# Performance work log

Hardware: AMD Instinct MI355X
Metric: run time of the kernel (lower is better)

The kernel has to match this reference:

```python
import jax, jax.numpy as jnp
import numpy as np

N_USERS = 100000
N_ITEMS = 50000
N = N_USERS + N_ITEMS
NNZ = 2400000
D = 64
L = 3
B = 16384


def setup_inputs() -> dict:
    key = jax.random.key(0)
    ks = jax.random.split(key, 12)
    return {
        "user_emb": jax.random.normal(ks[0], (N_USERS, D), jnp.float32) * 0.1,
        "item_emb": jax.random.normal(ks[1], (N_ITEMS, D), jnp.float32) * 0.1,
        "W_gc": jax.random.normal(ks[2], (L, D, D), jnp.float32) * 0.1,
        "b_gc": jax.random.normal(ks[3], (L, 1, D), jnp.float32) * 0.1,
        "W_bi": jax.random.normal(ks[4], (L, D, D), jnp.float32) * 0.1,
        "b_bi": jax.random.normal(ks[5], (L, 1, D), jnp.float32) * 0.1,
        "adj_vals": jax.random.uniform(ks[6], (NNZ,), jnp.float32) * (1.0 / 16.0),
        "adj_rows": jax.random.randint(ks[7], (NNZ,), 0, N, jnp.int32),
        "adj_cols": jax.random.randint(ks[8], (NNZ,), 0, N, jnp.int32),
        "u": jax.random.randint(ks[9], (B,), 0, N_USERS, jnp.int32),
        "i": jax.random.randint(ks[10], (B,), 0, N_ITEMS, jnp.int32),
        "j": jax.random.randint(ks[11], (B,), 0, N_ITEMS, jnp.int32),
    }


def reference(user_emb, item_emb, W_gc, b_gc, W_bi, b_bi, adj_vals, adj_rows, adj_cols, u, i, j):
    n_users = user_emb.shape[0]
    n_nodes = n_users + item_emb.shape[0]
    ego = jnp.concatenate([user_emb, item_emb], axis=0)  # [N, D]
    all_emb = [ego]
    n_layers = W_gc.shape[0]
    for l in range(n_layers):
        # spmm: side = A_hat @ ego  (edge-list gather + weighted segment sum)
        gathered = ego[adj_cols] * adj_vals[:, None]            # [nnz, D]
        side = jax.ops.segment_sum(gathered, adj_rows, num_segments=n_nodes)  # [N, D]
        # graph-conv branch
        sum_emb = jax.nn.leaky_relu(side @ W_gc[l] + b_gc[l], 0.2)
        # bi-interaction branch
        bi_emb = jax.nn.leaky_relu((ego * side) @ W_bi[l] + b_bi[l], 0.2)
        ego = sum_emb + bi_emb
        # L2 normalize per node (F.normalize, eps=1e-12)
        norm = ego / jnp.maximum(jnp.linalg.norm(ego, axis=1, keepdims=True), 1e-12)
        all_emb.append(norm)
    final = jnp.concatenate(all_emb, axis=1)  # [N, D*(L+1)]
    u_g = final[u]
    i_g = final[n_users + i]
    j_g = final[n_users + j]
    return u_g, i_g, j_g
```

## Files before the change

### kernel.cpp

```cpp
#include <hip/hip_runtime.h>

#define DD 64
#define RB 256
#define RB_SHIFT 8
#define CAP 4608
#define NBLKA 512
#define NBLKA_SHIFT 9
#define BMAX 1024
#define COLM 0x3FFFF
#define WT_STRIDE 80
#define EMAX 4704
#define SPAD 68

typedef __attribute__((ext_vector_type(8))) short bf16x8;
typedef __attribute__((ext_vector_type(4))) float f32x4;

static __device__ __forceinline__ float leaky(float x) {
    return x > 0.f ? x : 0.2f * x;
}

static __device__ __forceinline__ unsigned short f2bf(float f) {
    unsigned u = __float_as_uint(f);
    unsigned r = 0x7FFFu + ((u >> 16) & 1u);
    return (unsigned short)((u + r) >> 16);
}
#define BF_LO(w) __int_as_float((int)((w) << 16))
#define BF_HI(w) __int_as_float((int)((w) & 0xFFFF0000u))

static __device__ __forceinline__ bf16x8 pack8(float a, float b, float c, float d,
                                               float e, float f, float g, float h) {
    bf16x8 r;
    r[0] = (short)f2bf(a); r[1] = (short)f2bf(b); r[2] = (short)f2bf(c); r[3] = (short)f2bf(d);
    r[4] = (short)f2bf(e); r[5] = (short)f2bf(f); r[6] = (short)f2bf(g); r[7] = (short)f2bf(h);
    return r;
}

__global__ void concat_kernel(const float4* __restrict__ ue, const float4* __restrict__ ie,
                              float4* __restrict__ ego, ushort4* __restrict__ egob,
                              int n_user4, int total4) {
    int idx = blockIdx.x * blockDim.x + threadIdx.x;
    if (idx >= total4) return;
    float4 v = (idx < n_user4) ? ue[idx] : ie[idx - n_user4];
    ego[idx] = v;
    ushort4 b;
    b.x = f2bf(v.x); b.y = f2bf(v.y); b.z = f2bf(v.z); b.w = f2bf(v.w);
    egob[idx] = b;
}

__global__ void wtrans_kernel(const float* __restrict__ W, ushort* __restrict__ Wt) {
    __shared__ ushort t[64][65];
    const float* src = W + (size_t)blockIdx.x * 4096;
    ushort* dst = Wt + (size_t)blockIdx.x * 4096;
    int tid = threadIdx.x;
    for (int i = tid; i < 4096; i += 256) {
        int k = i >> 6, c = i & 63;
        t[k][c] = f2bf(src[i]);
    }
    __syncthreads();
    for (int i = tid; i < 4096; i += 256) {
        int c = i >> 6, k = i & 63;
        dst[i] = t[k][c];
    }
}

__global__ void bhist_kernel(const int* __restrict__ rows, int* __restrict__ counts_t, int nnz,
                             int nbuckets) {
    __shared__ int h[BMAX];
    int tid = threadIdx.x, blk = blockIdx.x;
    for (int i = tid; i < nbuckets; i += 256) h[i] = 0;
    __syncthreads();
    int chunk = (nnz + NBLKA - 1) / NBLKA;
    int lo = blk * chunk, hi = min(nnz, lo + chunk);
    for (int e = lo + tid; e < hi; e += 256) atomicAdd(&h[rows[e] >> RB_SHIFT], 1);
    __syncthreads();
    for (int i = tid; i < nbuckets; i += 256) counts_t[blk * nbuckets + i] = h[i];
}

__global__ void scan1_kernel(const int* __restrict__ counts_t, int* __restrict__ offsets,
                             int* __restrict__ blocksums, int flat, int nbuckets) {
    __shared__ int tmp[1024];
    int t = threadIdx.x;
    int g = blockIdx.x * 1024 + t;
    int x = 0;
    if (g < flat) {
        int i = g >> NBLKA_SHIFT, blk = g & (NBLKA - 1);
        x = counts_t[blk * nbuckets + i];
    }
    tmp[t] = x;
    __syncthreads();
    for (int off = 1; off < 1024; off <<= 1) {
        int y = (t >= off) ? tmp[t - off] : 0;
        __syncthreads();
        tmp[t] += y;
        __syncthreads();
    }
    if (g < flat) offsets[g + 1] = tmp[t];
    if (t == 1023) blocksums[blockIdx.x] = tmp[t];
    if (g == 0) offsets[0] = 0;
}

__global__ void scan2_kernel(int* blocksums, int nb) {
    __shared__ int tmp[1024];
    int t = threadIdx.x;
    int v = (t < nb) ? blocksums[t] : 0;
    tmp[t] = v;
    __syncthreads();
    for (int off = 1; off < 1024; off <<= 1) {
        int y = (t >= off) ? tmp[t - off] : 0;
        __syncthreads();
        tmp[t] += y;
        __syncthreads();
    }
    if (t < nb) blocksums[t] = tmp[t] - v;
}

__global__ void scan3_kernel(int* __restrict__ offsets, const int* __restrict__ blocksums,
                             int n) {
    int g = blockIdx.x * 1024 + threadIdx.x;
    if (g < n) offsets[g + 1] += blocksums[blockIdx.x];
}

__global__ void __launch_bounds__(256) bscatter_kernel(
    const int* __restrict__ rows, const int* __restrict__ cols,
    const float* __restrict__ vals, const int* __restrict__ offsets,
    int2* __restrict__ csr_cv, int nnz, int nbuckets) {
    __shared__ int hist[BMAX];
    __shared__ int lbase[BMAX];
    __shared__ int cur[BMAX];
    __shared__ int gcur[BMAX];
    __shared__ int tsum[256];
    __shared__ int2 buf[EMAX];
    __shared__ int dst[EMAX];
    int tid = threadIdx.x, blk = blockIdx.x;
    int chunk = (nnz + NBLKA - 1) / NBLKA;
    int lo = blk * chunk, hi = min(nnz, lo + chunk);
    for (int i = tid; i < BMAX; i += 256)
        gcur[i] = (i < nbuckets) ? offsets[i * NBLKA + blk] : 0;
    for (int sub = lo; sub < hi; sub += EMAX) {
        int scount = min(EMAX, hi - sub);
        for (int i = tid; i < BMAX; i += 256) hist[i] = 0;
        __syncthreads();
        for (int e = sub + tid; e < sub + scount; e += 256)
            atomicAdd(&hist[rows[e] >> RB_SHIFT], 1);
        __syncthreads();
        int loc[4];
        int s = 0;
        int bi = tid * 4;
#pragma unroll
        for (int j = 0; j < 4; ++j) { loc[j] = s; s += hist[bi + j]; }
        tsum[tid] = s;
        __syncthreads();
        for (int off = 1; off < 256; off <<= 1) {
            int v = (tid >= off) ? tsum[tid - off] : 0;
            __syncthreads();
            tsum[tid] += v;
            __syncthreads();
        }
        int excl = tid ? tsum[tid - 1] : 0;
#pragma unroll
        for (int j = 0; j < 4; ++j) {
            lbase[bi + j] = excl + loc[j];
            cur[bi + j] = excl + loc[j];
        }
        __syncthreads();
        for (int e = sub + tid; e < sub + scount; e += 256) {
            int r = rows[e];
            int b = r >> RB_SHIFT;
            int p = atomicAdd(&cur[b], 1);
            int2 cv;
            cv.x = ((r & (RB - 1)) << 18) | cols[e];
            cv.y = __float_as_int(vals[e]);
            buf[p] = cv;
            dst[p] = gcur[b] + (p - lbase[b]);
        }
        __syncthreads();
        for (int k = tid; k < scount; k += 256) csr_cv[dst[k]] = buf[k];
        __syncthreads();
        for (int i = tid; i < BMAX; i += 256) gcur[i] += hist[i];
        __syncthreads();
    }
}

__global__ void __launch_bounds__(256) sort_kernel(
    const int* __restrict__ offsets, const int2* __restrict__ csr_cv,
    int2* __restrict__ sorted_cv, int* __restrict__ rowoff_g, int nnz, int nbuckets) {
    __shared__ int2 sorted[CAP];
    __shared__ int hist[RB];
    __shared__ int rowoff[RB + 1];
    __shared__ int cur[RB];
    int tid = threadIdx.x;
    int b = blockIdx.x;
    int s = offsets[b * NBLKA];
    int e = offsets[(b + 1) * NBLKA];
    int m = e - s;

    hist[tid] = 0;
    __syncthreads();
    for (int k = s + tid; k < e; k += 256)
        atomicAdd(&hist[((unsigned)csr_cv[k].x) >> 18], 1);
    __syncthreads();
    for (int off = 1; off < RB; off <<= 1) {
        int v = (tid >= off) ? hist[tid - off] : 0;
        __syncthreads();
        hist[tid] += v;
        __syncthreads();
    }
    rowoff[tid + 1] = hist[tid];
    if (tid == 0) rowoff[0] = 0;
    __syncthreads();
    cur[tid] = rowoff[tid];
    __syncthreads();
    if (m <= CAP) {
        for (int k = s + tid; k < e; k += 256) {
            int2 cv = csr_cv[k];
            int p = atomicAdd(&cur[((unsigned)cv.x) >> 18], 1);
            sorted[p] = cv;
        }
        __syncthreads();
        for (int k = tid; k < m; k += 256) sorted_cv[s + k] = sorted[k];
    } else {
        for (int k = s + tid; k < e; k += 256) {
            int2 cv = csr_cv[k];
            int p = atomicAdd(&cur[((unsigned)cv.x) >> 18], 1);
            sorted_cv[s + p] = cv;
        }
    }
    rowoff_g[b * RB + tid] = s + rowoff[tid];
    if (b == 0 && tid == 0) rowoff_g[nbuckets * RB] = nnz;
}

#define EDGE8(acc, cvy, g)                                                     \
    do {                                                                       \
        float v_ = __int_as_float(cvy);                                        \
        acc[0] += v_ * BF_LO((g).x); acc[1] += v_ * BF_HI((g).x);              \
        acc[2] += v_ * BF_LO((g).y); acc[3] += v_ * BF_HI((g).y);              \
        acc[4] += v_ * BF_LO((g).z); acc[5] += v_ * BF_HI((g).z);              \
        acc[6] += v_ * BF_LO((g).w); acc[7] += v_ * BF_HI((g).w);              \
    } while (0)

__global__ void __launch_bounds__(512, 8) fused_layer_kernel(
    const uint4* __restrict__ egob_old, const float* __restrict__ ego_old,
    float* __restrict__ ego_new, ushort* __restrict__ egob_new,
    const int* __restrict__ rowoff, const int2* __restrict__ sorted_cv,
    const ushort* __restrict__ Wtg, const float* __restrict__ bgc,
    const ushort* __restrict__ Wtb, const float* __restrict__ bbi, int n) {
    __shared__ __align__(16) float sideL[64 * SPAD];
    __shared__ __align__(16) ushort sWg[DD * WT_STRIDE];
    __shared__ __align__(16) ushort sWb[DD * WT_STRIDE];
    int tid = threadIdx.x;
    for (int idx = tid; idx < DD * DD / 4; idx += 512) {
        int c = idx >> 4, k4 = idx & 15;
        *(ushort4*)&sWg[c * WT_STRIDE + k4 * 4] = ((const ushort4*)Wtg)[idx];
        *(ushort4*)&sWb[c * WT_STRIDE + k4 * 4] = ((const ushort4*)Wtb)[idx];
    }
    int base64 = blockIdx.x * 64;
    int wave = tid >> 6, lane = tid & 63;
    int sub = lane >> 3, l8 = lane & 7;

    int lr0 = wave * 8 + sub;
    int row0 = base64 + lr0;
    float acc0[8] = {0.f, 0.f, 0.f, 0.f, 0.f, 0.f, 0.f, 0.f};
    int k0 = 0, E0 = 0;
    if (row0 < n) { k0 = rowoff[row0]; E0 = rowoff[row0 + 1]; }
    int CL0 = (E0 > 0) ? E0 - 1 : 0;

    int myit = (E0 - k0 + 3) >> 2;
    myit = max(myit, __shfl_xor(myit, 8, 64));
    myit = max(myit, __shfl_xor(myit, 16, 64));
    myit = max(myit, __shfl_xor(myit, 32, 64));

    int2 cA0[4];
#pragma unroll
    for (int j = 0; j < 4; ++j) {
        int i0 = k0 + j; cA0[j] = sorted_cv[i0 < E0 ? i0 : CL0];
    }
    for (int it = 0; it < myit; ++it) {
        uint4 g0[4];
#pragma unroll
        for (int j = 0; j < 4; ++j)
            g0[j] = egob_old[(unsigned)(cA0[j].x & COLM) * 8 + l8];
        int2 cB0[4];
#pragma unroll
        for (int j = 0; j < 4; ++j) {
            int i0 = k0 + 4 + j; cB0[j] = sorted_cv[i0 < E0 ? i0 : CL0];
        }
#pragma unroll
        for (int j = 0; j < 4; ++j) {
            int vb0 = (k0 + j < E0) ? cA0[j].y : 0;
            EDGE8(acc0, vb0, g0[j]);
        }
        k0 += 4;
#pragma unroll
        for (int j = 0; j < 4; ++j) cA0[j] = cB0[j];
    }
    {
        float4 o0 = {acc0[0], acc0[1], acc0[2], acc0[3]};
        float4 o1 = {acc0[4], acc0[5], acc0[6], acc0[7]};
        *(float4*)&sideL[lr0 * SPAD + l8 * 8] = o0;
        *(float4*)&sideL[lr0 * SPAD + l8 * 8 + 4] = o1;
    }
    __syncthreads();

    int m = lane & 15, quad = lane >> 4;
    int wr = wave >> 1, ch = wave & 1;
    int lr = wr * 16 + m;
    int base = base64 + wr * 16;
    int rowc = min(base64 + lr, n - 1);

    float4 s0 = *(const float4*)&sideL[lr * SPAD + quad * 8];
    float4 s1 = *(const float4*)&sideL[lr * SPAD + quad * 8 + 4];
    float4 s2 = *(const float4*)&sideL[lr * SPAD + 32 + quad * 8];
    float4 s3 = *(const float4*)&sideL[lr * SPAD + 32 + quad * 8 + 4];
    const float4* erow = (const float4*)(ego_old + (size_t)rowc * DD);
    float4 e0 = erow[quad * 2], e1 = erow[quad * 2 + 1];
    float4 e2 = erow[8 + quad * 2], e3 = erow[8 + quad * 2 + 1];

    bf16x8 aS_lo = pack8(s0.x, s0.y, s0.z, s0.w, s1.x, s1.y, s1.z, s1.w);
    bf16x8 aS_hi = pack8(s2.x, s2.y, s2.z, s2.w, s3.x, s3.y, s3.z, s3.w);
    bf16x8 aP_lo = pack8(e0.x * s0.x, e0.y * s0.y, e0.z * s0.z, e0.w * s0.w,
                         e1.x * s1.x, e1.y * s1.y, e1.z * s1.z, e1.w * s1.w);
    bf16x8 aP_hi = pack8(e2.x * s2.x, e2.y * s2.y, e2.z * s2.z, e2.w * s2.w,
                         e3.x * s3.x, e3.y * s3.y, e3.z * s3.z, e3.w * s3.w);

#pragma unroll
    for (int cti = 0; cti < 2; ++cti) {
        int ct = ch * 2 + cti;
        int col = ct * 16 + m;
        bf16x8 bg_lo = *(const bf16x8*)&sWg[col * WT_STRIDE + quad * 8];
        bf16x8 bg_hi = *(const bf16x8*)&sWg[col * WT_STRIDE + 32 + quad * 8];
        bf16x8 bb_lo = *(const bf16x8*)&sWb[col * WT_STRIDE + quad * 8];
        bf16x8 bb_hi = *(const bf16x8*)&sWb[col * WT_STRIDE + 32 + quad * 8];
        f32x4 accG = (f32x4){0.f, 0.f, 0.f, 0.f};
        f32x4 accB = (f32x4){0.f, 0.f, 0.f, 0.f};
        accG = __builtin_amdgcn_mfma_f32_16x16x32_bf16(aS_lo, bg_lo, accG, 0, 0, 0);
        accG = __builtin_amdgcn_mfma_f32_16x16x32_bf16(aS_hi, bg_hi, accG, 0, 0, 0);
        accB = __builtin_amdgcn_mfma_f32_16x16x32_bf16(aP_lo, bb_lo, accB, 0, 0, 0);
        accB = __builtin_amdgcn_mfma_f32_16x16x32_bf16(aP_hi, bb_hi, accB, 0, 0, 0);
        float bg = bgc[col], bb = bbi[col];
#pragma unroll
        for (int r = 0; r < 4; ++r) {
            int node = base + quad * 4 + r;
            if (node < n) {
                float o = leaky(accG[r] + bg) + leaky(accB[r] + bb);
                ego_new[(size_t)node * DD + col] = o;
                egob_new[(size_t)node * DD + col] = f2bf(o);
            }
        }
    }
}

__global__ void gather_kernel(const float* __restrict__ ego, const int* __restrict__ u,
                              const int* __restrict__ ii, const int* __restrict__ jj,
                              float* __restrict__ out, int layer, int B, int n_users,
                              int normalize) {
    int wid = (blockIdx.x * blockDim.x + threadIdx.x) >> 6;
    int lane = threadIdx.x & 63;
    if (wid >= 3 * B) return;
    int arr = wid / B;
    int b = wid - arr * B;
    int node = (arr == 0) ? u[b] : ((arr == 1) ? n_users + ii[b] : n_users + jj[b]);
    float v = ego[node * DD + lane];
    if (normalize) {
        float ss = v * v;
#pragma unroll
        for (int m = 32; m; m >>= 1) ss += __shfl_xor(ss, m, 64);
        v /= fmaxf(sqrtf(ss), 1e-12f);
    }
    out[wid * 256 + layer * DD + lane] = v;
}

extern "C" void kernel_launch(void* const* d_in, const int* in_sizes, int n_in,
                              void* d_out, int out_size, void* d_ws, size_t ws_size,
                              hipStream_t stream) {
    const float* user_emb = (const float*)d_in[0];
    const float* item_emb = (const float*)d_in[1];
    const float* W_gc = (const float*)d_in[2];
    const float* b_gc = (const float*)d_in[3];
    const float* W_bi = (const float*)d_in[4];
    const float* b_bi = (const float*)d_in[5];
    const float* adj_vals = (const float*)d_in[6];
    const int* adj_rows = (const int*)d_in[7];
    const int* adj_cols = (const int*)d_in[8];
    const int* u = (const int*)d_in[9];
    const int* ii = (const int*)d_in[10];
    const int* jj = (const int*)d_in[11];
    float* out = (float*)d_out;

    const int D = DD;
    int n_users = in_sizes[0] / D;
    int n_items = in_sizes[1] / D;
    int n = n_users + n_items;
    int nnz = in_sizes[6];
    int B = in_sizes[9];
    int L = in_sizes[2] / (D * D);

    int nbuckets = (n + RB - 1) / RB;
    int flat = nbuckets * NBLKA;

    char* ws = (char*)d_ws;
    auto alloc = [&](size_t bytes) {
        char* p = ws;
        ws += (bytes + 255) & ~(size_t)255;
        return p;
    };
    float* ego_a = (float*)alloc((size_t)n * D * 4);
    float* ego_b = (float*)alloc((size_t)n * D * 4);
    ushort* egob_a = (ushort*)alloc((size_t)n * D * 2);
    ushort* egob_b = (ushort*)alloc((size_t)n * D * 2);
    int* counts_t = (int*)alloc((size_t)flat * 4);
    int* offsets = (int*)alloc((size_t)(flat + 1) * 4);
    int* blocksums = (int*)alloc(4096);
    int2* csr_cv = (int2*)alloc((size_t)nnz * 8);
    int2* sorted_cv = (int2*)alloc((size_t)nnz * 8);
    int* rowoff = (int*)alloc((size_t)(nbuckets * RB + 1) * 4);
    ushort* wt_g = (ushort*)alloc((size_t)L * D * D * 2);
    ushort* wt_b = (ushort*)alloc((size_t)L * D * D * 2);

    int total4 = n * D / 4, nu4 = n_users * D / 4;
    concat_kernel<<<(total4 + 255) / 256, 256, 0, stream>>>(
        (const float4*)user_emb, (const float4*)item_emb, (float4*)ego_a, (ushort4*)egob_a,
        nu4, total4);

    wtrans_kernel<<<L, 256, 0, stream>>>(W_gc, wt_g);
    wtrans_kernel<<<L, 256, 0, stream>>>(W_bi, wt_b);

    int grows = 3 * B;
    gather_kernel<<<(grows + 3) / 4, 256, 0, stream>>>(ego_a, u, ii, jj, out, 0, B, n_users, 0);

    bhist_kernel<<<NBLKA, 256, 0, stream>>>(adj_rows, counts_t, nnz, nbuckets);
    int nblk1 = (flat + 1023) / 1024;
    scan1_kernel<<<nblk1, 1024, 0, stream>>>(counts_t, offsets, blocksums, flat, nbuckets);
    scan2_kernel<<<1, 1024, 0, stream>>>(blocksums, nblk1);
    scan3_kernel<<<nblk1, 1024, 0, stream>>>(offsets, blocksums, flat);
    bscatter_kernel<<<NBLKA, 256, 0, stream>>>(adj_rows, adj_cols, adj_vals, offsets, csr_cv,
                                               nnz, nbuckets);
    sort_kernel<<<nbuckets, 256, 0, stream>>>(offsets, csr_cv, sorted_cv, rowoff, nnz, nbuckets);

    float* eo = ego_a; ushort* ebo = egob_a;
    float* en = ego_b; ushort* ebn = egob_b;
    int fblocks = (n + 63) / 64;
    for (int l = 0; l < L; ++l) {
        fused_layer_kernel<<<fblocks, 512, 0, stream>>>(
            (const uint4*)ebo, eo, en, ebn, rowoff, sorted_cv,
            wt_g + (size_t)l * D * D, b_gc + (size_t)l * D,
            wt_b + (size_t)l * D * D, b_bi + (size_t)l * D, n);
        gather_kernel<<<(grows + 3) / 4, 256, 0, stream>>>(en, u, ii, jj, out, l + 1, B,
                                                           n_users, 1);
        float* tf = eo; eo = en; en = tf;
        ushort* tb = ebo; ebo = ebn; ebn = tb;
    }
}
```

Measured before the change: 455.5 us.

## Merge preprocessing launches and fold output gathers into fused layer kernels

The concat and two weight-transpose kernels become one launch. The three-stage per-block offset scan is replaced by global bucket totals accumulated with atomics, a single small scan, and per-sub-chunk atomic cursor reservation in the scatter. The gather of each layer's previous embeddings moves into extra blocks of the next fused layer kernel, so fewer kernels run serially. The trade-offs are that bucket placement is no longer deterministic (atomic cursor ordering) and gather blocks share the grid with the heavier layer blocks.

```diff
diff --git a/kernel.cpp b/kernel.cpp
--- a/kernel.cpp
+++ b/kernel.cpp
@@ -5,7 +5,6 @@
 #define RB_SHIFT 8
 #define CAP 4608
 #define NBLKA 512
-#define NBLKA_SHIFT 9
 #define BMAX 1024
 #define COLM 0x3FFFF
 #define WT_STRIDE 80
@@ -35,10 +34,32 @@
     return r;
 }
 
-__global__ void concat_kernel(const float4* __restrict__ ue, const float4* __restrict__ ie,
-                              float4* __restrict__ ego, ushort4* __restrict__ egob,
-                              int n_user4, int total4) {
-    int idx = blockIdx.x * blockDim.x + threadIdx.x;
+__global__ void concat_wtrans_kernel(const float4* __restrict__ ue,
+                                     const float4* __restrict__ ie,
+                                     float4* __restrict__ ego, ushort4* __restrict__ egob,
+                                     int n_user4, int total4, int cblocks,
+                                     const float* __restrict__ Wg, const float* __restrict__ Wb,
+                                     ushort* __restrict__ wtg, ushort* __restrict__ wtb, int L) {
+    __shared__ ushort t[64][65];
+    int tid = threadIdx.x;
+    if ((int)blockIdx.x >= cblocks) {
+        int which = blockIdx.x - cblocks;
+        const float* src = (which < L) ? Wg + (size_t)which * 4096
+                                       : Wb + (size_t)(which - L) * 4096;
+        ushort* dst = (which < L) ? wtg + (size_t)which * 4096
+                                  : wtb + (size_t)(which - L) * 4096;
+        for (int i = tid; i < 4096; i += 256) {
+            int k = i >> 6, c = i & 63;
+            t[k][c] = f2bf(src[i]);
+        }
+        __syncthreads();
+        for (int i = tid; i < 4096; i += 256) {
+            int c = i >> 6, k = i & 63;
+            dst[i] = t[k][c];
+        }
+        return;
+    }
+    int idx = blockIdx.x * 256 + tid;
     if (idx >= total4) return;
     float4 v = (idx < n_user4) ? ue[idx] : ie[idx - n_user4];
     ego[idx] = v;
@@ -47,24 +68,8 @@
     egob[idx] = b;
 }
 
-__global__ void wtrans_kernel(const float* __restrict__ W, ushort* __restrict__ Wt) {
-    __shared__ ushort t[64][65];
-    const float* src = W + (size_t)blockIdx.x * 4096;
-    ushort* dst = Wt + (size_t)blockIdx.x * 4096;
-    int tid = threadIdx.x;
-    for (int i = tid; i < 4096; i += 256) {
-        int k = i >> 6, c = i & 63;
-        t[k][c] = f2bf(src[i]);
-    }
-    __syncthreads();
-    for (int i = tid; i < 4096; i += 256) {
-        int c = i >> 6, k = i & 63;
-        dst[i] = t[k][c];
-    }
-}
-
-__global__ void bhist_kernel(const int* __restrict__ rows, int* __restrict__ counts_t, int nnz,
-                             int nbuckets) {
+__global__ void bhist2_kernel(const int* __restrict__ rows, int* __restrict__ btotal,
+                              int nnz, int nbuckets) {
     __shared__ int h[BMAX];
     int tid = threadIdx.x, blk = blockIdx.x;
     for (int i = tid; i < nbuckets; i += 256) h[i] = 0;
@@ -73,20 +78,16 @@
     int lo = blk * chunk, hi = min(nnz, lo + chunk);
     for (int e = lo + tid; e < hi; e += 256) atomicAdd(&h[rows[e] >> RB_SHIFT], 1);
     __syncthreads();
-    for (int i = tid; i < nbuckets; i += 256) counts_t[blk * nbuckets + i] = h[i];
-}
-
-__global__ void scan1_kernel(const int* __restrict__ counts_t, int* __restrict__ offsets,
-                             int* __restrict__ blocksums, int flat, int nbuckets) {
+    for (int i = tid; i < nbuckets; i += 256)
+        if (h[i]) atomicAdd(&btotal[i], h[i]);
+}
+
+__global__ void bscan_kernel(const int* __restrict__ btotal, int* __restrict__ base,
+                             int* __restrict__ cursor, int nb) {
     __shared__ int tmp[1024];
     int t = threadIdx.x;
-    int g = blockIdx.x * 1024 + t;
-    int x = 0;
-    if (g < flat) {
-        int i = g >> NBLKA_SHIFT, blk = g & (NBLKA - 1);
-        x = counts_t[blk * nbuckets + i];
-    }
-    tmp[t] = x;
+    int v = (t < nb) ? btotal[t] : 0;
+    tmp[t] = v;
     __syncthreads();
     for (int off = 1; off < 1024; off <<= 1) {
         int y = (t >= off) ? tmp[t - off] : 0;
@@ -94,35 +95,16 @@
         tmp[t] += y;
         __syncthreads();
     }
-    if (g < flat) offsets[g + 1] = tmp[t];
-    if (t == 1023) blocksums[blockIdx.x] = tmp[t];
-    if (g == 0) offsets[0] = 0;
-}
-
-__global__ void scan2_kernel(int* blocksums, int nb) {
-    __shared__ int tmp[1024];
-    int t = threadIdx.x;
-    int v = (t < nb) ? blocksums[t] : 0;
-    tmp[t] = v;
-    __syncthreads();
-    for (int off = 1; off < 1024; off <<= 1) {
-        int y = (t >= off) ? tmp[t - off] : 0;
-        __syncthreads();
-        tmp[t] += y;
-        __syncthreads();
-    }
-    if (t < nb) blocksums[t] = tmp[t] - v;
-}
-
-__global__ void scan3_kernel(int* __restrict__ offsets, const int* __restrict__ blocksums,
-                             int n) {
-    int g = blockIdx.x * 1024 + threadIdx.x;
-    if (g < n) offsets[g + 1] += blocksums[blockIdx.x];
+    if (t < nb) {
+        base[t + 1] = tmp[t];
+        cursor[t] = tmp[t] - v;
+    }
+    if (t == 0) base[0] = 0;
 }
 
 __global__ void __launch_bounds__(256) bscatter_kernel(
     const int* __restrict__ rows, const int* __restrict__ cols,
-    const float* __restrict__ vals, const int* __restrict__ offsets,
+    const float* __restrict__ vals, int* __restrict__ cursor,
     int2* __restrict__ csr_cv, int nnz, int nbuckets) {
     __shared__ int hist[BMAX];
     __shared__ int lbase[BMAX];
@@ -134,8 +116,6 @@
     int tid = threadIdx.x, blk = blockIdx.x;
     int chunk = (nnz + NBLKA - 1) / NBLKA;
     int lo = blk * chunk, hi = min(nnz, lo + chunk);
-    for (int i = tid; i < BMAX; i += 256)
-        gcur[i] = (i < nbuckets) ? offsets[i * NBLKA + blk] : 0;
     for (int sub = lo; sub < hi; sub += EMAX) {
         int scount = min(EMAX, hi - sub);
         for (int i = tid; i < BMAX; i += 256) hist[i] = 0;
@@ -159,8 +139,10 @@
         int excl = tid ? tsum[tid - 1] : 0;
 #pragma unroll
         for (int j = 0; j < 4; ++j) {
-            lbase[bi + j] = excl + loc[j];
-            cur[bi + j] = excl + loc[j];
+            int b = bi + j;
+            lbase[b] = excl + loc[j];
+            cur[b] = excl + loc[j];
+            if (hist[b] > 0) gcur[b] = atomicAdd(&cursor[b], hist[b]);
         }
         __syncthreads();
         for (int e = sub + tid; e < sub + scount; e += 256) {
@@ -176,13 +158,11 @@
         __syncthreads();
         for (int k = tid; k < scount; k += 256) csr_cv[dst[k]] = buf[k];
         __syncthreads();
-        for (int i = tid; i < BMAX; i += 256) gcur[i] += hist[i];
-        __syncthreads();
     }
 }
 
 __global__ void __launch_bounds__(256) sort_kernel(
-    const int* __restrict__ offsets, const int2* __restrict__ csr_cv,
+    const int* __restrict__ base, const int2* __restrict__ csr_cv,
     int2* __restrict__ sorted_cv, int* __restrict__ rowoff_g, int nnz, int nbuckets) {
     __shared__ int2 sorted[CAP];
     __shared__ int hist[RB];
@@ -190,8 +170,8 @@
     __shared__ int cur[RB];
     int tid = threadIdx.x;
     int b = blockIdx.x;
-    int s = offsets[b * NBLKA];
-    int e = offsets[(b + 1) * NBLKA];
+    int s = base[b];
+    int e = base[b + 1];
     int m = e - s;
 
     hist[tid] = 0;
@@ -243,18 +223,40 @@
     float* __restrict__ ego_new, ushort* __restrict__ egob_new,
     const int* __restrict__ rowoff, const int2* __restrict__ sorted_cv,
     const ushort* __restrict__ Wtg, const float* __restrict__ bgc,
-    const ushort* __restrict__ Wtb, const float* __restrict__ bbi, int n) {
+    const ushort* __restrict__ Wtb, const float* __restrict__ bbi, int n,
+    int fblocks, const int* __restrict__ u, const int* __restrict__ ii,
+    const int* __restrict__ jj, float* __restrict__ out, int B, int n_users,
+    int glayer, int gnorm, int ostride) {
     __shared__ __align__(16) float sideL[64 * SPAD];
     __shared__ __align__(16) ushort sWg[DD * WT_STRIDE];
     __shared__ __align__(16) ushort sWb[DD * WT_STRIDE];
     int tid = threadIdx.x;
+    int wave = tid >> 6, lane = tid & 63;
+
+    if ((int)blockIdx.x >= fblocks) {
+        int wid = (blockIdx.x - fblocks) * 8 + wave;
+        if (wid < 3 * B) {
+            int arr = wid / B;
+            int b = wid - arr * B;
+            int node = (arr == 0) ? u[b] : ((arr == 1) ? n_users + ii[b] : n_users + jj[b]);
+            float v = ego_old[(size_t)node * DD + lane];
+            if (gnorm) {
+                float ss = v * v;
+#pragma unroll
+                for (int m = 32; m; m >>= 1) ss += __shfl_xor(ss, m, 64);
+                v /= fmaxf(sqrtf(ss), 1e-12f);
+            }
+            out[(size_t)wid * ostride + glayer * DD + lane] = v;
+        }
+        return;
+    }
+
     for (int idx = tid; idx < DD * DD / 4; idx += 512) {
         int c = idx >> 4, k4 = idx & 15;
         *(ushort4*)&sWg[c * WT_STRIDE + k4 * 4] = ((const ushort4*)Wtg)[idx];
         *(ushort4*)&sWb[c * WT_STRIDE + k4 * 4] = ((const ushort4*)Wtb)[idx];
     }
     int base64 = blockIdx.x * 64;
-    int wave = tid >> 6, lane = tid & 63;
     int sub = lane >> 3, l8 = lane & 7;
 
     int lr0 = wave * 8 + sub;
@@ -352,21 +354,21 @@
 __global__ void gather_kernel(const float* __restrict__ ego, const int* __restrict__ u,
                               const int* __restrict__ ii, const int* __restrict__ jj,
                               float* __restrict__ out, int layer, int B, int n_users,
-                              int normalize) {
+                              int normalize, int ostride) {
     int wid = (blockIdx.x * blockDim.x + threadIdx.x) >> 6;
     int lane = threadIdx.x & 63;
     if (wid >= 3 * B) return;
     int arr = wid / B;
     int b = wid - arr * B;
     int node = (arr == 0) ? u[b] : ((arr == 1) ? n_users + ii[b] : n_users + jj[b]);
-    float v = ego[node * DD + lane];
+    float v = ego[(size_t)node * DD + lane];
     if (normalize) {
         float ss = v * v;
 #pragma unroll
         for (int m = 32; m; m >>= 1) ss += __shfl_xor(ss, m, 64);
         v /= fmaxf(sqrtf(ss), 1e-12f);
     }
-    out[wid * 256 + layer * DD + lane] = v;
+    out[(size_t)wid * ostride + layer * DD + lane] = v;
 }
 
 extern "C" void kernel_launch(void* const* d_in, const int* in_sizes, int n_in,
@@ -393,9 +395,9 @@
     int nnz = in_sizes[6];
     int B = in_sizes[9];
     int L = in_sizes[2] / (D * D);
+    int ostride = (L + 1) * D;
 
     int nbuckets = (n + RB - 1) / RB;
-    int flat = nbuckets * NBLKA;
 
     char* ws = (char*)d_ws;
     auto alloc = [&](size_t bytes) {
@@ -407,46 +409,44 @@
     float* ego_b = (float*)alloc((size_t)n * D * 4);
     ushort* egob_a = (ushort*)alloc((size_t)n * D * 2);
     ushort* egob_b = (ushort*)alloc((size_t)n * D * 2);
-    int* counts_t = (int*)alloc((size_t)flat * 4);
-    int* offsets = (int*)alloc((size_t)(flat + 1) * 4);
-    int* blocksums = (int*)alloc(4096);
+    int* btotal = (int*)alloc((size_t)(nbuckets + 1) * 4);
+    int* bbase = (int*)alloc((size_t)(nbuckets + 1) * 4);
+    int* bcursor = (int*)alloc((size_t)(nbuckets + 1) * 4);
     int2* csr_cv = (int2*)alloc((size_t)nnz * 8);
     int2* sorted_cv = (int2*)alloc((size_t)nnz * 8);
     int* rowoff = (int*)alloc((size_t)(nbuckets * RB + 1) * 4);
     ushort* wt_g = (ushort*)alloc((size_t)L * D * D * 2);
     ushort* wt_b = (ushort*)alloc((size_t)L * D * D * 2);
 
+    hipMemsetAsync(btotal, 0, (size_t)(nbuckets + 1) * 4, stream);
+
     int total4 = n * D / 4, nu4 = n_users * D / 4;
-    concat_kernel<<<(total4 + 255) / 256, 256, 0, stream>>>(
+    int cblocks = (total4 + 255) / 256;
+    concat_wtrans_kernel<<<cblocks + 2 * L, 256, 0, stream>>>(
         (const float4*)user_emb, (const float4*)item_emb, (float4*)ego_a, (ushort4*)egob_a,
-        nu4, total4);
-
-    wtrans_kernel<<<L, 256, 0, stream>>>(W_gc, wt_g);
-    wtrans_kernel<<<L, 256, 0, stream>>>(W_bi, wt_b);
-
-    int grows = 3 * B;
-    gather_kernel<<<(grows + 3) / 4, 256, 0, stream>>>(ego_a, u, ii, jj, out, 0, B, n_users, 0);
-
-    bhist_kernel<<<NBLKA, 256, 0, stream>>>(adj_rows, counts_t, nnz, nbuckets);
-    int nblk1 = (flat + 1023) / 1024;
-    scan1_kernel<<<nblk1, 1024, 0, stream>>>(counts_t, offsets, blocksums, flat, nbuckets);
-    scan2_kernel<<<1, 1024, 0, stream>>>(blocksums, nblk1);
-    scan3_kernel<<<nblk1, 1024, 0, stream>>>(offsets, blocksums, flat);
-    bscatter_kernel<<<NBLKA, 256, 0, stream>>>(adj_rows, adj_cols, adj_vals, offsets, csr_cv,
+        nu4, total4, cblocks, W_gc, W_bi, wt_g, wt_b, L);
+
+    bhist2_kernel<<<NBLKA, 256, 0, stream>>>(adj_rows, btotal, nnz, nbuckets);
+    bscan_kernel<<<1, 1024, 0, stream>>>(btotal, bbase, bcursor, nbuckets);
+    bscatter_kernel<<<NBLKA, 256, 0, stream>>>(adj_rows, adj_cols, adj_vals, bcursor, csr_cv,
                                                nnz, nbuckets);
-    sort_kernel<<<nbuckets, 256, 0, stream>>>(offsets, csr_cv, sorted_cv, rowoff, nnz, nbuckets);
+    sort_kernel<<<nbuckets, 256, 0, stream>>>(bbase, csr_cv, sorted_cv, rowoff, nnz, nbuckets);
 
     float* eo = ego_a; ushort* ebo = egob_a;
     float* en = ego_b; ushort* ebn = egob_b;
     int fblocks = (n + 63) / 64;
+    int grows = 3 * B;
+    int gblocks = (grows + 7) / 8;
     for (int l = 0; l < L; ++l) {
-        fused_layer_kernel<<<fblocks, 512, 0, stream>>>(
+        fused_layer_kernel<<<fblocks + gblocks, 512, 0, stream>>>(
             (const uint4*)ebo, eo, en, ebn, rowoff, sorted_cv,
             wt_g + (size_t)l * D * D, b_gc + (size_t)l * D,
-            wt_b + (size_t)l * D * D, b_bi + (size_t)l * D, n);
-        gather_kernel<<<(grows + 3) / 4, 256, 0, stream>>>(en, u, ii, jj, out, l + 1, B,
-                                                           n_users, 1);
+            wt_b + (size_t)l * D * D, b_bi + (size_t)l * D, n,
+            fblocks, u, ii, jj, out, B, n_users, l, (l > 0) ? 1 : 0, ostride);
         float* tf = eo; eo = en; en = tf;
         ushort* tb = ebo; ebo = ebn; ebn = tb;
     }
-}
+
+    gather_kernel<<<(grows + 3) / 4, 256, 0, stream>>>(eo, u, ii, jj, out, L, B, n_users, 1,
+                                                       ostride);
+}
```

Result: no change. 464.3 us (+1.9%).
